# Performance work log

Hardware: AMD Instinct MI355X
Metric: run time of the kernel (lower is better)

## Reference

```python
import jax, jax.numpy as jnp
import numpy as np

N_NODES = 50000
N_EDGES = 800000
HIDDEN = 128
BN_EPS = 1e-5
LEAKY_SLOPE = 0.01


def setup_inputs() -> dict:
    key = jax.random.key(0)
    ks = jax.random.split(key, 8)
    x = jax.random.normal(ks[0], (N_NODES, HIDDEN), dtype=jnp.float32)
    edge_index = jax.random.randint(ks[1], (2, N_EDGES), 0, N_NODES, dtype=jnp.int64)
    # stacked per-layer params (4 SAGEConv layers, all 128->128)
    sc = 1.0 / np.sqrt(HIDDEN)
    Wl = jax.random.normal(ks[2], (4, HIDDEN, HIDDEN), dtype=jnp.float32) * sc
    bl = jax.random.normal(ks[3], (4, HIDDEN), dtype=jnp.float32) * sc
    Wr = jax.random.normal(ks[4], (4, HIDDEN, HIDDEN), dtype=jnp.float32) * sc
    gamma = jnp.ones((4, HIDDEN), dtype=jnp.float32)
    beta = jnp.zeros((4, HIDDEN), dtype=jnp.float32)
    return {"x": x, "edge_index": edge_index, "Wl": Wl, "bl": bl,
            "Wr": Wr, "gamma": gamma, "beta": beta}


def _sage_mean_agg(x, src, dst, n):
    # gather source features per edge, scatter-mean onto destination nodes
    msg = x[src]                                                  # [E, F]
    agg = jax.ops.segment_sum(msg, dst, num_segments=n)           # [N, F]
    cnt = jax.ops.segment_sum(jnp.ones_like(dst, dtype=x.dtype), dst, num_segments=n)
    return agg / jnp.maximum(cnt, 1.0)[:, None]


def _bn_train(x, g, b):
    mu = jnp.mean(x, axis=0)
    var = jnp.mean((x - mu) ** 2, axis=0)  # biased variance (PyTorch BN normalization)
    return (x - mu) * jax.lax.rsqrt(var + BN_EPS) * g + b


def reference(x, edge_index, Wl, bl, Wr, gamma, beta):
    src, dst = edge_index[0], edge_index[1]
    n = x.shape[0]
    h = x
    for i in range(4):
        agg = _sage_mean_agg(h, src, dst, n)
        h = agg @ Wl[i] + bl[i] + h @ Wr[i]          # SAGEConv: lin_l(mean_nbr) + lin_r(root)
        h = jnp.where(h >= 0, h, LEAKY_SLOPE * h)    # leaky_relu
        h = _bn_train(h, gamma[i], beta[i])
    # dropout: eval-mode identity (deterministic reference)
    return h
```

## Files before the change

### kernel.cpp

```cpp
#include <hip/hip_runtime.h>
#include <hip/hip_bf16.h>

#define N_NODES 50000
#define N_EDGES 800000
#define F 128
#define BN_EPS 1e-5f
#define SLOPE 0.01f
#define NB 782
#define CAP 64
#define NBIN 128
#define BINSZ 391
#define QCAP2 8192
#define ABLK 512
#define AITER 7
#define PB1 6250
#define PB2 512

#define SLABR 50048
#define SLABST (SLABR * 32)
#define ZROW 50000
#define AGG_K 391
#define AGG_GRID (8 * AGG_K)

typedef __attribute__((ext_vector_type(8))) __bf16 bf16x8_t;
typedef __attribute__((ext_vector_type(8))) unsigned short u16x8_t;
typedef __attribute__((ext_vector_type(4))) float f32x4_t;

__device__ __forceinline__ unsigned short f2b(float f) {
    unsigned int u = __float_as_uint(f);
    unsigned int r = (u + 0x7fffu + ((u >> 16) & 1u)) >> 16;
    return (unsigned short)r;
}
__device__ __forceinline__ float b2f_lo(unsigned int v) { return __uint_as_float(v << 16); }
__device__ __forceinline__ float b2f_hi(unsigned int v) { return __uint_as_float(v & 0xffff0000u); }


__global__ __launch_bounds__(256) void bucket2_kernel(const int* __restrict__ src,
                                                      const int* __restrict__ dst,
                                                      int* __restrict__ qtail,
                                                      unsigned int* __restrict__ qdata) {
    __shared__ int counts[NBIN];
    __shared__ int cur[NBIN];
    __shared__ int base[NBIN];
    const int tid = threadIdx.x;

    for (int k = tid; k < NBIN; k += 256) { counts[k] = 0; cur[k] = 0; }
    __syncthreads();

    unsigned int pack[AITER];
    int bin[AITER];
    const int stride = ABLK * 256;
#pragma unroll
    for (int it = 0; it < AITER; ++it) {
        const int e = blockIdx.x * 256 + tid + it * stride;
        bin[it] = -1;
        if (e < N_EDGES) {
            int d = __builtin_nontemporal_load(dst + e);
            int s = __builtin_nontemporal_load(src + e);
            bin[it] = d / BINSZ;
            pack[it] = ((unsigned int)d << 16) | (unsigned int)s;
            atomicAdd(&counts[bin[it]], 1);
        }
    }
    __syncthreads();
    if (tid < NBIN) {
        int c = counts[tid];
        base[tid] = (c > 0) ? atomicAdd(&qtail[tid * 16], c) : 0;
    }
    __syncthreads();
#pragma unroll
    for (int it = 0; it < AITER; ++it) {
        if (bin[it] >= 0) {
            int slot = base[bin[it]] + atomicAdd(&cur[bin[it]], 1);
            qdata[(long)bin[it] * QCAP2 + slot] = pack[it];
        }
    }
}

__global__ __launch_bounds__(256) void scatter2_kernel(const unsigned int* __restrict__ qdata,
                                                       const int* __restrict__ qtail,
                                                       int* __restrict__ deg,
                                                       unsigned short* __restrict__ csr) {
    __shared__ int cnt[BINSZ];
    __shared__ __align__(16) unsigned short stage[BINSZ][CAP];
    const int b = blockIdx.x;
    const int nbase = b * BINSZ;
    const int nn = min(BINSZ, N_NODES - nbase);
    const int tid = threadIdx.x;

    for (int r = tid; r < BINSZ; r += 256) cnt[r] = 0;
    __syncthreads();

    const int n = qtail[b * 16];
    const unsigned int* q = qdata + (long)b * QCAP2;
    for (int i = tid; i < n; i += 256) {
        unsigned int p = q[i];
        int local = (int)(p >> 16) - nbase;
        int pos = atomicAdd(&cnt[local], 1);
        if (pos < CAP) stage[local][pos] = (unsigned short)(p & 0xffff);
    }
    __syncthreads();

    for (int c = tid; c < nn * (CAP / 8); c += 256) {
        const int r = c >> 3;
        const int col = (c & 7) * 8;
        *(u16x8_t*)(csr + (long)(nbase + r) * CAP + col) = *(const u16x8_t*)&stage[r][col];
    }
    for (int r = tid; r < nn; r += 256) deg[nbase + r] = min(cnt[r], CAP);
}


__global__ __launch_bounds__(256) void prep_kernel(const float* __restrict__ x,
                                                   unsigned short* __restrict__ hbA,
                                                   unsigned short* __restrict__ hbB,
                                                   const float* __restrict__ Wl,
                                                   const float* __restrict__ Wr,
                                                   unsigned short* __restrict__ Wt,
                                                   float* __restrict__ scale,
                                                   float* __restrict__ shift) {
    const int b = blockIdx.x;
    const int tid = threadIdx.x;
    if (b < PB1) {
        long i = (long)b * 256 + tid;
        const int node = (int)(i >> 5);
        const int j = (int)(i & 31);
        const int s = j >> 3;
        const int cj = j & 7;
        float4 v = ((const float4*)x)[i];
        ushort4 o;
        o.x = f2b(v.x); o.y = f2b(v.y); o.z = f2b(v.z); o.w = f2b(v.w);
        ((ushort4*)hbA)[(long)s * (SLABR * 8) + (long)node * 8 + cj] = o;
    } else if (b < PB1 + PB2) {
        int idx = (b - PB1) * 256 + tid;
        int k = idx & 255;
        int n = (idx >> 8) & 127;
        int i = idx >> 15;
        float v = (k < F) ? Wl[((long)i * F + k) * F + n]
                          : Wr[((long)i * F + (k - F)) * F + n];
        Wt[idx] = f2b(v);
    } else {
        if (tid < F) { scale[tid] = 1.f; shift[tid] = 0.f; }
        else if (tid < 160) {
            int t = tid - 128;
            ushort4 z; z.x = 0; z.y = 0; z.z = 0; z.w = 0;
            ((ushort4*)hbA)[(long)(t >> 3) * (SLABR * 8) + (long)ZROW * 8 + (t & 7)] = z;
            ((ushort4*)hbB)[(long)(t >> 3) * (SLABR * 8) + (long)ZROW * 8 + (t & 7)] = z;
        }
    }
}


#define ACC8(A, V)                               \
    A[0] += b2f_lo(V.x); A[1] += b2f_hi(V.x);    \
    A[2] += b2f_lo(V.y); A[3] += b2f_hi(V.y);    \
    A[4] += b2f_lo(V.z); A[5] += b2f_hi(V.z);    \
    A[6] += b2f_lo(V.w); A[7] += b2f_hi(V.w);

__global__ __launch_bounds__(256) void agg_slab(const unsigned short* __restrict__ hb,
                                                const int* __restrict__ deg,
                                                const unsigned short* __restrict__ csr,
                                                const float* __restrict__ scale,
                                                const float* __restrict__ shift,
                                                unsigned short* __restrict__ aggs) {
    const int b = blockIdx.x;
    const int xcd = b & 7;
    const int slab = xcd & 3;
    const int range = (b >> 3) * 2 + (xcd >> 2);
    const int tid = threadIdx.x;
    const int wave = tid >> 6, lane = tid & 63;
    const int n = lane >> 2;
    const int c = lane & 3;

    const int node = range * 64 + wave * 16 + n;
    const bool nval = node < N_NODES;
    const int nodec = nval ? node : (N_NODES - 1);

    const unsigned short* hs = hb + (long)slab * SLABST + c * 8;
    const unsigned short* crow = csr + (long)nodec * CAP;
    const int d = nval ? deg[nodec] : 0;

    int dmax = d;
    dmax = max(dmax, __shfl_xor(dmax, 4));
    dmax = max(dmax, __shfl_xor(dmax, 8));
    dmax = max(dmax, __shfl_xor(dmax, 16));
    dmax = max(dmax, __shfl_xor(dmax, 32));

    float a[8];
#pragma unroll
    for (int j = 0; j < 8; ++j) a[j] = 0.f;

    for (int e0 = 0; e0 < dmax; e0 += 4) {
        const ushort4 iv = *(const ushort4*)(crow + e0);
        const int i0 = (e0 < d) ? (int)iv.x : ZROW;
        const int i1 = (e0 + 1 < d) ? (int)iv.y : ZROW;
        const int i2 = (e0 + 2 < d) ? (int)iv.z : ZROW;
        const int i3 = (e0 + 3 < d) ? (int)iv.w : ZROW;
        const uint4 v0 = *(const uint4*)(hs + (long)i0 * 32);
        const uint4 v1 = *(const uint4*)(hs + (long)i1 * 32);
        const uint4 v2 = *(const uint4*)(hs + (long)i2 * 32);
        const uint4 v3 = *(const uint4*)(hs + (long)i3 * 32);
        ACC8(a, v0);
        ACC8(a, v1);
        ACC8(a, v2);
        ACC8(a, v3);
    }

    if (nval) {
        u16x8_t o;
        if (d > 0) {
            const float inv = 1.0f / (float)d;
            const int fb = slab * 32 + c * 8;
            const float4 sc0 = *(const float4*)(scale + fb);
            const float4 sc1 = *(const float4*)(scale + fb + 4);
            const float4 sh0 = *(const float4*)(shift + fb);
            const float4 sh1 = *(const float4*)(shift + fb + 4);
            o[0] = f2b(a[0] * inv * sc0.x + sh0.x);
            o[1] = f2b(a[1] * inv * sc0.y + sh0.y);
            o[2] = f2b(a[2] * inv * sc0.z + sh0.z);
            o[3] = f2b(a[3] * inv * sc0.w + sh0.w);
            o[4] = f2b(a[4] * inv * sc1.x + sh1.x);
            o[5] = f2b(a[5] * inv * sc1.y + sh1.y);
            o[6] = f2b(a[6] * inv * sc1.z + sh1.z);
            o[7] = f2b(a[7] * inv * sc1.w + sh1.w);
        } else {
#pragma unroll
            for (int j = 0; j < 8; ++j) o[j] = 0;
        }
        *(u16x8_t*)(aggs + (long)slab * SLABST + (long)node * 32 + c * 8) = o;
    }
}

__device__ __forceinline__ u16x8_t affine8(u16x8_t av, const float* __restrict__ sc,
                                           const float* __restrict__ sh) {
    u16x8_t r;
#pragma unroll
    for (int j = 0; j < 8; ++j) {
        float v = __uint_as_float(((unsigned int)av[j]) << 16);
        v = v * sc[j] + sh[j];
        r[j] = f2b(v);
    }
    return r;
}

#if __has_builtin(__builtin_amdgcn_global_load_lds)
#define STAGE_HALF(half) {                                                        \
    _Pragma("unroll")                                                             \
    for (int f = 0; f < 8; ++f) {                                                 \
        const int fid = f * 256 + tid;                                            \
        const int lf = fid & 63;                                                  \
        const int ksf = (fid >> 6) & 3;                                           \
        const int ntf = fid >> 8;                                                 \
        const int n = ntf * 16 + (lf & 15);                                       \
        const int k = (half) * 128 + ksf * 32 + (lf >> 4) * 8;                    \
        const unsigned short* gsrc = Wt + (long)n * 256 + k;                      \
        unsigned short* lbase = stage + (f * 256 + wave * 64) * 8;                \
        __builtin_amdgcn_global_load_lds(                                         \
            (const __attribute__((address_space(1))) void*)gsrc,                  \
            (__attribute__((address_space(3))) void*)lbase, 16, 0, 0);            \
    } }
#else
#define STAGE_HALF(half) {                                                        \
    _Pragma("unroll")                                                             \
    for (int f = 0; f < 8; ++f) {                                                 \
        const int fid = f * 256 + tid;                                            \
        const int lf = fid & 63;                                                  \
        const int ksf = (fid >> 6) & 3;                                           \
        const int ntf = fid >> 8;                                                 \
        const int n = ntf * 16 + (lf & 15);                                       \
        const int k = (half) * 128 + ksf * 32 + (lf >> 4) * 8;                    \
        const unsigned short* gsrc = Wt + (long)n * 256 + k;                      \
        *(u16x8_t*)(stage + fid * 8) = *(const u16x8_t*)gsrc;                     \
    } }
#endif

__global__ __launch_bounds__(256) void gemm_mfma(const unsigned short* __restrict__ aggs,
                                                 const unsigned short* __restrict__ hin,
                                                 const float* __restrict__ scale,
                                                 const float* __restrict__ shift,
                                                 const unsigned short* __restrict__ Wt,
                                                 const float* __restrict__ bl,
                                                 unsigned short* __restrict__ Pb,
                                                 float* __restrict__ partial) {
    __shared__ __align__(16) char shraw[32768];
    unsigned short* stage = (unsigned short*)shraw;
    unsigned short* ep16 = (unsigned short*)shraw;
    __shared__ float lsum[4][F];
    __shared__ float lsq[4][F];

    const int tid = threadIdx.x;
    const int wave = tid >> 6, lane = tid & 63;
    const int m = lane & 15, q = lane >> 4;
    const int rbase = blockIdx.x * 64 + wave * 16;
    const int arow = rbase + m;
    const bool aval = arow < N_NODES;

    u16x8_t areg[8];
#pragma unroll
    for (int j = 0; j < 8; ++j) areg[j] = (u16x8_t)0;
    if (aval) {
#pragma unroll
        for (int j = 0; j < 4; ++j)
            areg[j] = *(const u16x8_t*)(aggs + (long)j * SLABST + (long)arow * 32 + q * 8);
#pragma unroll
        for (int j = 0; j < 4; ++j) {
            u16x8_t raw = *(const u16x8_t*)(hin + (long)j * SLABST + (long)arow * 32 + q * 8);
            const int base = j * 32 + q * 8;
            areg[4 + j] = affine8(raw, scale + base, shift + base);
        }
    }

    f32x4_t acc[8];
#pragma unroll
    for (int nt = 0; nt < 8; ++nt) acc[nt] = (f32x4_t){0.f, 0.f, 0.f, 0.f};

    for (int half = 0; half < 2; ++half) {
        if (half) __syncthreads();
        STAGE_HALF(half);
        __syncthreads();
#pragma unroll
        for (int ks = 0; ks < 4; ++ks) {
            bf16x8_t af = __builtin_bit_cast(bf16x8_t, areg[half * 4 + ks]);
#pragma unroll
            for (int nt = 0; nt < 8; ++nt) {
                u16x8_t bv = *(const u16x8_t*)(stage + ((nt * 4 + ks) * 64 + lane) * 8);
                bf16x8_t bf = __builtin_bit_cast(bf16x8_t, bv);
                acc[nt] = __builtin_amdgcn_mfma_f32_16x16x32_bf16(af, bf, acc[nt], 0, 0, 0);
            }
        }
    }

    __syncthreads();

    float cs[8], cq[8];
#pragma unroll
    for (int nt = 0; nt < 8; ++nt) {
        cs[nt] = 0.f; cq[nt] = 0.f;
        const int c = nt * 16 + m;
        const float b = bl[c];
#pragma unroll
        for (int r = 0; r < 4; ++r) {
            const int rl = wave * 16 + q * 4 + r;
            float v = acc[nt][r] + b;
            v = (v >= 0.f) ? v : SLOPE * v;
            ep16[rl * 136 + c] = f2b(v);
            if (rbase + q * 4 + r < N_NODES) {
                cs[nt] += v;
                cq[nt] += v * v;
            }
        }
    }

    {
        const int rq = lane >> 4;
        const int ch = lane & 15;
        const int s = ch >> 2;
        const int cw = ch & 3;
#pragma unroll
        for (int r2 = 0; r2 < 4; ++r2) {
            const int rl = wave * 16 + rq * 4 + r2;
            const int grow = blockIdx.x * 64 + rl;
            if (grow < N_NODES)
                *(u16x8_t*)(Pb + (long)s * SLABST + (long)grow * 32 + cw * 8) =
                    *(const u16x8_t*)(ep16 + rl * 136 + ch * 8);
        }
    }

#pragma unroll
    for (int nt = 0; nt < 8; ++nt) {
        cs[nt] += __shfl_xor(cs[nt], 16);
        cs[nt] += __shfl_xor(cs[nt], 32);
        cq[nt] += __shfl_xor(cq[nt], 16);
        cq[nt] += __shfl_xor(cq[nt], 32);
    }
    if (lane < 16) {
#pragma unroll
        for (int nt = 0; nt < 8; ++nt) {
            lsum[wave][nt * 16 + m] = cs[nt];
            lsq[wave][nt * 16 + m] = cq[nt];
        }
    }
    __syncthreads();
    if (tid < F) {
        float s = 0.f, s2 = 0.f;
#pragma unroll
        for (int w = 0; w < 4; ++w) {
            s += lsum[w][tid];
            s2 += lsq[w][tid];
        }
        partial[(long)blockIdx.x * 256 + tid] = s;
        partial[(long)blockIdx.x * 256 + 128 + tid] = s2;
    }
}

__global__ __launch_bounds__(256) void bn_reduce(const float* __restrict__ partial,
                                                 const float* __restrict__ gamma,
                                                 const float* __restrict__ beta,
                                                 float* __restrict__ scale,
                                                 float* __restrict__ shift) {
    const int j = blockIdx.x;
    const int t = threadIdx.x;
    const int lane = t & 63, wave = t >> 6;
    float s = 0.f, s2 = 0.f;
    for (int b = t; b < NB; b += 256) {
        s += partial[(long)b * 256 + j];
        s2 += partial[(long)b * 256 + 128 + j];
    }
#pragma unroll
    for (int off = 1; off < 64; off <<= 1) {
        s += __shfl_xor(s, off);
        s2 += __shfl_xor(s2, off);
    }
    __shared__ float ls[4], lq[4];
    if (lane == 0) { ls[wave] = s; lq[wave] = s2; }
    __syncthreads();
    if (t == 0) {
        float S = ls[0] + ls[1] + ls[2] + ls[3];
        float Q = lq[0] + lq[1] + lq[2] + lq[3];
        const float inv_n = 1.0f / (float)N_NODES;
        float mu = S * inv_n;
        float var = Q * inv_n - mu * mu;
        float scl = gamma[j] * rsqrtf(var + BN_EPS);
        scale[j] = scl;
        shift[j] = beta[j] - mu * scl;
    }
}

__global__ __launch_bounds__(256) void bn_apply_f(const unsigned short* __restrict__ Pb,
                                                  float* __restrict__ out,
                                                  const float* __restrict__ scale,
                                                  const float* __restrict__ shift) {
    long i = (long)blockIdx.x * blockDim.x + threadIdx.x;
    if (i >= (long)N_NODES * (F / 8)) return;
    const int node = (int)(i >> 4);
    const int c8 = (int)(i & 15);
    const int s = c8 >> 2;
    const int cw = c8 & 3;
    uint4 v = *(const uint4*)(Pb + (long)s * SLABST + (long)node * 32 + cw * 8);
    const float4 sc0 = ((const float4*)scale)[c8 * 2];
    const float4 sc1 = ((const float4*)scale)[c8 * 2 + 1];
    const float4 sh0 = ((const float4*)shift)[c8 * 2];
    const float4 sh1 = ((const float4*)shift)[c8 * 2 + 1];
    float4 o0, o1;
    o0.x = b2f_lo(v.x) * sc0.x + sh0.x;
    o0.y = b2f_hi(v.x) * sc0.y + sh0.y;
    o0.z = b2f_lo(v.y) * sc0.z + sh0.z;
    o0.w = b2f_hi(v.y) * sc0.w + sh0.w;
    o1.x = b2f_lo(v.z) * sc1.x + sh1.x;
    o1.y = b2f_hi(v.z) * sc1.y + sh1.y;
    o1.z = b2f_lo(v.w) * sc1.z + sh1.z;
    o1.w = b2f_hi(v.w) * sc1.w + sh1.w;
    ((float4*)out)[i * 2] = o0;
    ((float4*)out)[i * 2 + 1] = o1;
}


extern "C" void kernel_launch(void* const* d_in, const int* in_sizes, int n_in,
                              void* d_out, int out_size, void* d_ws, size_t ws_size,
                              hipStream_t stream) {
    const float* x     = (const float*)d_in[0];
    const int*   ei    = (const int*)d_in[1];
    const float* Wl    = (const float*)d_in[2];
    const float* bl    = (const float*)d_in[3];
    const float* Wr    = (const float*)d_in[4];
    const float* gamma = (const float*)d_in[5];
    const float* beta  = (const float*)d_in[6];
    float* out = (float*)d_out;

    const int* src = ei;
    const int* dst = ei + N_EDGES;

    char* w = (char*)d_ws;
    auto alloc = [&](size_t bytes) -> char* {
        char* p = w;
        w += (bytes + 255) & ~(size_t)255;
        return p;
    };
    unsigned short* hbA   = (unsigned short*)alloc((size_t)4 * SLABST * 2);
    unsigned short* hbB   = (unsigned short*)alloc((size_t)4 * SLABST * 2);
    unsigned short* aggb  = (unsigned short*)alloc((size_t)4 * SLABST * 2);
    unsigned short* Wt    = (unsigned short*)alloc((size_t)4 * F * 256 * 2);
    int*   deg      = (int*)alloc((size_t)N_NODES * 4);
    int*   qtail    = (int*)alloc((size_t)NBIN * 16 * 4);
    unsigned int* qdata = (unsigned int*)alloc((size_t)NBIN * QCAP2 * 4);
    unsigned short* csr = (unsigned short*)alloc((size_t)SLABR * CAP * 2);
    float* partial  = (float*)alloc((size_t)NB * 256 * 4);
    float* scale    = (float*)alloc(F * 4);
    float* shift    = (float*)alloc(F * 4);

    hipMemsetAsync(qtail, 0, (size_t)NBIN * 16 * 4, stream);

    bucket2_kernel<<<ABLK, 256, 0, stream>>>(src, dst, qtail, qdata);
    scatter2_kernel<<<NBIN, 256, 0, stream>>>(qdata, qtail, deg, csr);
    prep_kernel<<<PB1 + PB2 + 1, 256, 0, stream>>>(x, hbA, hbB, Wl, Wr, Wt, scale, shift);

    const int n8 = N_NODES * (F / 8);

    unsigned short* hin = hbA;
    unsigned short* hnext = hbB;
    for (int i = 0; i < 4; ++i) {
        agg_slab<<<AGG_GRID, 256, 0, stream>>>(hin, deg, csr, scale, shift, aggb);

        gemm_mfma<<<NB, 256, 0, stream>>>(
            aggb, hin, scale, shift, Wt + (size_t)i * F * 256, bl + (size_t)i * F,
            hnext, partial);

        bn_reduce<<<F, 256, 0, stream>>>(partial, gamma + (size_t)i * F, beta + (size_t)i * F,
                                         scale, shift);

        unsigned short* t = hin; hin = hnext; hnext = t;
    }
    bn_apply_f<<<(n8 + 255) / 256, 256, 0, stream>>>(hin, out, scale, shift);
}
```

Baseline: 370.0 us.

## Fuse BN reduction into GEMM via last-block pattern and stage full weight tile

Folds the separate per-layer BatchNorm reduction kernel into the GEMM kernel. Each block bumps an atomic counter, and the last block to finish reduces all partial sums and writes the new scale and shift. The GEMM block grows to 512 threads covering 128 rows and stages the whole 256-wide weight tile into LDS once, instead of in two halves with extra barriers. This removes four kernel launches and halves the partial-sum count, at the cost of a serialized tail reduction in one block, higher LDS use per block, and fewer blocks per CU.

```diff
diff --git a/kernel.cpp b/kernel.cpp
--- a/kernel.cpp
+++ b/kernel.cpp
@@ -6,7 +6,7 @@
 #define F 128
 #define BN_EPS 1e-5f
 #define SLOPE 0.01f
-#define NB 782
+#define NB 391
 #define CAP 64
 #define NBIN 128
 #define BINSZ 391
@@ -243,56 +243,64 @@
 }
 
 #if __has_builtin(__builtin_amdgcn_global_load_lds)
-#define STAGE_HALF(half) {                                                        \
+#define STAGE_ALL() {                                                             \
     _Pragma("unroll")                                                             \
     for (int f = 0; f < 8; ++f) {                                                 \
-        const int fid = f * 256 + tid;                                            \
+        const int fid = f * 512 + tid;                                            \
         const int lf = fid & 63;                                                  \
-        const int ksf = (fid >> 6) & 3;                                           \
-        const int ntf = fid >> 8;                                                 \
+        const int ksf = (fid >> 6) & 7;                                           \
+        const int ntf = fid >> 9;                                                 \
         const int n = ntf * 16 + (lf & 15);                                       \
-        const int k = (half) * 128 + ksf * 32 + (lf >> 4) * 8;                    \
+        const int k = ksf * 32 + (lf >> 4) * 8;                                   \
         const unsigned short* gsrc = Wt + (long)n * 256 + k;                      \
-        unsigned short* lbase = stage + (f * 256 + wave * 64) * 8;                \
+        unsigned short* lbase = stage + (f * 512 + wave * 64) * 8;                \
         __builtin_amdgcn_global_load_lds(                                         \
             (const __attribute__((address_space(1))) void*)gsrc,                  \
             (__attribute__((address_space(3))) void*)lbase, 16, 0, 0);            \
     } }
 #else
-#define STAGE_HALF(half) {                                                        \
+#define STAGE_ALL() {                                                             \
     _Pragma("unroll")                                                             \
     for (int f = 0; f < 8; ++f) {                                                 \
-        const int fid = f * 256 + tid;                                            \
+        const int fid = f * 512 + tid;                                            \
         const int lf = fid & 63;                                                  \
-        const int ksf = (fid >> 6) & 3;                                           \
-        const int ntf = fid >> 8;                                                 \
+        const int ksf = (fid >> 6) & 7;                                           \
+        const int ntf = fid >> 9;                                                 \
         const int n = ntf * 16 + (lf & 15);                                       \
-        const int k = (half) * 128 + ksf * 32 + (lf >> 4) * 8;                    \
+        const int k = ksf * 32 + (lf >> 4) * 8;                                   \
         const unsigned short* gsrc = Wt + (long)n * 256 + k;                      \
         *(u16x8_t*)(stage + fid * 8) = *(const u16x8_t*)gsrc;                     \
     } }
 #endif
 
-__global__ __launch_bounds__(256) void gemm_mfma(const unsigned short* __restrict__ aggs,
+__global__ __launch_bounds__(512) void gemm_mfma(const unsigned short* __restrict__ aggs,
                                                  const unsigned short* __restrict__ hin,
                                                  const float* __restrict__ scale,
                                                  const float* __restrict__ shift,
                                                  const unsigned short* __restrict__ Wt,
                                                  const float* __restrict__ bl,
+                                                 const float* __restrict__ gamma,
+                                                 const float* __restrict__ beta,
                                                  unsigned short* __restrict__ Pb,
-                                                 float* __restrict__ partial) {
-    __shared__ __align__(16) char shraw[32768];
+                                                 float* __restrict__ partial,
+                                                 float* __restrict__ nscale,
+                                                 float* __restrict__ nshift,
+                                                 int* __restrict__ counter) {
+    __shared__ __align__(16) char shraw[65536];
     unsigned short* stage = (unsigned short*)shraw;
     unsigned short* ep16 = (unsigned short*)shraw;
-    __shared__ float lsum[4][F];
-    __shared__ float lsq[4][F];
+    __shared__ float lsum[8][F];
+    __shared__ float lsq[8][F];
+    __shared__ int lastFlag;
 
     const int tid = threadIdx.x;
     const int wave = tid >> 6, lane = tid & 63;
     const int m = lane & 15, q = lane >> 4;
-    const int rbase = blockIdx.x * 64 + wave * 16;
+    const int rbase = blockIdx.x * 128 + wave * 16;
     const int arow = rbase + m;
     const bool aval = arow < N_NODES;
+
+    STAGE_ALL();
 
     u16x8_t areg[8];
 #pragma unroll
@@ -313,19 +321,15 @@
 #pragma unroll
     for (int nt = 0; nt < 8; ++nt) acc[nt] = (f32x4_t){0.f, 0.f, 0.f, 0.f};
 
-    for (int half = 0; half < 2; ++half) {
-        if (half) __syncthreads();
-        STAGE_HALF(half);
-        __syncthreads();
-#pragma unroll
-        for (int ks = 0; ks < 4; ++ks) {
-            bf16x8_t af = __builtin_bit_cast(bf16x8_t, areg[half * 4 + ks]);
-#pragma unroll
-            for (int nt = 0; nt < 8; ++nt) {
-                u16x8_t bv = *(const u16x8_t*)(stage + ((nt * 4 + ks) * 64 + lane) * 8);
-                bf16x8_t bf = __builtin_bit_cast(bf16x8_t, bv);
-                acc[nt] = __builtin_amdgcn_mfma_f32_16x16x32_bf16(af, bf, acc[nt], 0, 0, 0);
-            }
+    __syncthreads();
+#pragma unroll
+    for (int ks = 0; ks < 8; ++ks) {
+        bf16x8_t af = __builtin_bit_cast(bf16x8_t, areg[ks]);
+#pragma unroll
+        for (int nt = 0; nt < 8; ++nt) {
+            u16x8_t bv = *(const u16x8_t*)(stage + ((nt * 8 + ks) * 64 + lane) * 8);
+            bf16x8_t bf = __builtin_bit_cast(bf16x8_t, bv);
+            acc[nt] = __builtin_amdgcn_mfma_f32_16x16x32_bf16(af, bf, acc[nt], 0, 0, 0);
         }
     }
 
@@ -358,7 +362,7 @@
 #pragma unroll
         for (int r2 = 0; r2 < 4; ++r2) {
             const int rl = wave * 16 + rq * 4 + r2;
-            const int grow = blockIdx.x * 64 + rl;
+            const int grow = blockIdx.x * 128 + rl;
             if (grow < N_NODES)
                 *(u16x8_t*)(Pb + (long)s * SLABST + (long)grow * 32 + cw * 8) =
                     *(const u16x8_t*)(ep16 + rl * 136 + ch * 8);
@@ -383,46 +387,43 @@
     if (tid < F) {
         float s = 0.f, s2 = 0.f;
 #pragma unroll
-        for (int w = 0; w < 4; ++w) {
+        for (int w = 0; w < 8; ++w) {
             s += lsum[w][tid];
             s2 += lsq[w][tid];
         }
         partial[(long)blockIdx.x * 256 + tid] = s;
         partial[(long)blockIdx.x * 256 + 128 + tid] = s2;
     }
-}
-
-__global__ __launch_bounds__(256) void bn_reduce(const float* __restrict__ partial,
-                                                 const float* __restrict__ gamma,
-                                                 const float* __restrict__ beta,
-                                                 float* __restrict__ scale,
-                                                 float* __restrict__ shift) {
-    const int j = blockIdx.x;
-    const int t = threadIdx.x;
-    const int lane = t & 63, wave = t >> 6;
-    float s = 0.f, s2 = 0.f;
-    for (int b = t; b < NB; b += 256) {
-        s += partial[(long)b * 256 + j];
-        s2 += partial[(long)b * 256 + 128 + j];
-    }
-#pragma unroll
-    for (int off = 1; off < 64; off <<= 1) {
-        s += __shfl_xor(s, off);
-        s2 += __shfl_xor(s2, off);
-    }
-    __shared__ float ls[4], lq[4];
-    if (lane == 0) { ls[wave] = s; lq[wave] = s2; }
-    __syncthreads();
-    if (t == 0) {
-        float S = ls[0] + ls[1] + ls[2] + ls[3];
-        float Q = lq[0] + lq[1] + lq[2] + lq[3];
+
+    __threadfence();
+    if (tid == 0) lastFlag = (atomicAdd(counter, 1) == (int)gridDim.x - 1);
+    __syncthreads();
+    if (!lastFlag) return;
+    __threadfence();
+
+    {
+        const int j = tid & 127;
+        const int part = tid >> 7;
+        float s = 0.f, s2 = 0.f;
+        for (int b = part; b < NB; b += 4) {
+            s += partial[(long)b * 256 + j];
+            s2 += partial[(long)b * 256 + 128 + j];
+        }
+        lsum[part][j] = s;
+        lsq[part][j] = s2;
+    }
+    __syncthreads();
+    if (tid < F) {
+        float S = lsum[0][tid] + lsum[1][tid] + lsum[2][tid] + lsum[3][tid];
+        float Q = lsq[0][tid] + lsq[1][tid] + lsq[2][tid] + lsq[3][tid];
         const float inv_n = 1.0f / (float)N_NODES;
         float mu = S * inv_n;
         float var = Q * inv_n - mu * mu;
-        float scl = gamma[j] * rsqrtf(var + BN_EPS);
-        scale[j] = scl;
-        shift[j] = beta[j] - mu * scl;
-    }
+        float scl = gamma[tid] * rsqrtf(var + BN_EPS);
+        nscale[tid] = scl;
+        nshift[tid] = beta[tid] - mu * scl;
+    }
+    if (tid == 0) *counter = 0;
 }
 
 __global__ __launch_bounds__(256) void bn_apply_f(const unsigned short* __restrict__ Pb,
@@ -481,13 +482,14 @@
     unsigned short* Wt    = (unsigned short*)alloc((size_t)4 * F * 256 * 2);
     int*   deg      = (int*)alloc((size_t)N_NODES * 4);
     int*   qtail    = (int*)alloc((size_t)NBIN * 16 * 4);
+    int*   counter  = (int*)alloc(256);
     unsigned int* qdata = (unsigned int*)alloc((size_t)NBIN * QCAP2 * 4);
     unsigned short* csr = (unsigned short*)alloc((size_t)SLABR * CAP * 2);
     float* partial  = (float*)alloc((size_t)NB * 256 * 4);
     float* scale    = (float*)alloc(F * 4);
     float* shift    = (float*)alloc(F * 4);
 
-    hipMemsetAsync(qtail, 0, (size_t)NBIN * 16 * 4, stream);
+    hipMemsetAsync(qtail, 0, (size_t)NBIN * 16 * 4 + 256, stream);
 
     bucket2_kernel<<<ABLK, 256, 0, stream>>>(src, dst, qtail, qdata);
     scatter2_kernel<<<NBIN, 256, 0, stream>>>(qdata, qtail, deg, csr);
@@ -500,12 +502,10 @@
     for (int i = 0; i < 4; ++i) {
         agg_slab<<<AGG_GRID, 256, 0, stream>>>(hin, deg, csr, scale, shift, aggb);
 
-        gemm_mfma<<<NB, 256, 0, stream>>>(
+        gemm_mfma<<<NB, 512, 0, stream>>>(
             aggb, hin, scale, shift, Wt + (size_t)i * F * 256, bl + (size_t)i * F,
-            hnext, partial);
-
-        bn_reduce<<<F, 256, 0, stream>>>(partial, gamma + (size_t)i * F, beta + (size_t)i * F,
-                                         scale, shift);
+            gamma + (size_t)i * F, beta + (size_t)i * F,
+            hnext, partial, scale, shift, counter);
 
         unsigned short* t = hin; hin = hnext; hnext = t;
     }
```

After: 631.9 us. +70.8%, slower.
